# Optimization experiments

Hardware: AMD Instinct MI355X
Metric: run time of the kernel (lower is better)

The kernel has to match this reference:

```python
import jax, jax.numpy as jnp
import numpy as np

WEIGHT = 0.1  # init weight

# 6-connectivity (scipy generate_binary_structure(3,1)) neighbor reductions

def _nmin(x, fill):
    p = jnp.pad(x, 1, constant_values=fill)
    return jnp.minimum(
        jnp.minimum(jnp.minimum(p[:-2, 1:-1, 1:-1], p[2:, 1:-1, 1:-1]),
                    jnp.minimum(p[1:-1, :-2, 1:-1], p[1:-1, 2:, 1:-1])),
        jnp.minimum(p[1:-1, 1:-1, :-2], p[1:-1, 1:-1, 2:]))


def _nor(x):
    p = jnp.pad(x, 1, constant_values=False)
    return (p[:-2, 1:-1, 1:-1] | p[2:, 1:-1, 1:-1] |
            p[1:-1, :-2, 1:-1] | p[1:-1, 2:, 1:-1] |
            p[1:-1, 1:-1, :-2] | p[1:-1, 1:-1, 2:])


def _nand(x):
    # border_value=0 in scipy.binary_erosion -> pad with False
    p = jnp.pad(x, 1, constant_values=False)
    return (p[:-2, 1:-1, 1:-1] & p[2:, 1:-1, 1:-1] &
            p[1:-1, :-2, 1:-1] & p[1:-1, 2:, 1:-1] &
            p[1:-1, 1:-1, :-2] & p[1:-1, 1:-1, 2:])


def _cc_count(mask):
    # connected-component count via min-label propagation (6-connectivity),
    # equivalent to scipy.ndimage.label(...)[1]
    n = mask.size
    idx = jnp.arange(n, dtype=jnp.int32).reshape(mask.shape)
    big = jnp.int32(n)
    lbl0 = jnp.where(mask, idx, big)

    def body(c):
        lbl, _ = c
        new = jnp.where(mask, jnp.minimum(lbl, _nmin(lbl, big)), big)
        return new, jnp.any(new != lbl)

    lbl, _ = jax.lax.while_loop(lambda c: c[1], body, (lbl0, jnp.bool_(True)))
    # roots: voxels whose label equals their own index
    return jnp.sum(mask & (lbl == idx)).astype(jnp.int32)


def _cavity_volume(mask):
    # binary_fill_holes: background not reachable from the border
    bg = ~mask
    border = jnp.ones(mask.shape, bool).at[1:-1, 1:-1, 1:-1].set(False)
    r0 = bg & border

    def body(c):
        r, _ = c
        new = bg & (r | _nor(r))
        return new, jnp.any(new != r)

    reach, _ = jax.lax.while_loop(lambda c: c[1], body, (r0, jnp.bool_(True)))
    return jnp.sum(bg & ~reach).astype(jnp.int32)


def _betti(mask):
    b0 = _cc_count(mask)
    eroded = mask & _nand(mask)  # binary_erosion, iterations=1
    b0e = _cc_count(eroded)
    b1 = jnp.maximum(jnp.int32(0), b0 - b0e)
    b2 = _cavity_volume(mask) // 100
    return jnp.stack([b0, b1, b2]).astype(jnp.float32)


def setup_inputs() -> dict:
    key = jax.random.key(0)
    k1, k2 = jax.random.split(key)
    B, C, D, H, W = 2, 4, 64, 128, 128
    pred = jax.random.normal(k1, (B, C, D, H, W), dtype=jnp.float32)
    target = jax.random.randint(k2, (B, D, H, W), 0, C, dtype=jnp.int32)
    return {"pred": pred, "target": target}


def reference(pred, target):
    B, C = pred.shape[0], pred.shape[1]
    vol = pred.shape[2:]
    prob = jax.nn.softmax(pred, axis=1)
    # foreground classes 1..C-1, flattened to [B*(C-1), D, H, W]
    pred_masks = (prob[:, 1:] > 0.5).reshape((-1,) + vol)
    cls = jnp.arange(1, C, dtype=target.dtype).reshape(1, C - 1, 1, 1, 1)
    tgt_masks = (target[:, None] == cls).reshape((-1,) + vol)
    pb = jax.vmap(_betti)(pred_masks)  # [B*(C-1), 3]
    tb = jax.vmap(_betti)(tgt_masks)
    count = B * (C - 1)
    return WEIGHT * jnp.abs(pb - tb).sum() / count
```

## Files before the change

kernel.cpp:

```cpp
#include <hip/hip_runtime.h>
#include <stdint.h>

#define DD 64
#define HH 128
#define WW 128
#define NVOX (DD * HH * WW)
#define NWRD (NVOX / 32)
#define BATCH 2
#define NCLS 4
#define NMASK 12
#define NPROB 36
#define NTILE 128
#define MAXC 2048
#define VNODE (NTILE * MAXC)
#define NODE_STRIDE (VNODE + 64)
#define NTASKW 7424

__device__ __forceinline__ int uf_find(int* P, int x) {
    while (true) {
        int p = P[x];
        if (p == x) return x;
        int gp = P[p];
        if (gp != p) P[x] = gp;
        x = gp;
    }
}
__device__ __forceinline__ int uf_find_ro(const int* P, int x) {
    int p;
    while ((p = P[x]) != x) x = p;
    return x;
}
__device__ __forceinline__ void uf_union(int* P, int a, int b) {
    while (true) {
        a = uf_find(P, a);
        b = uf_find(P, b);
        if (a == b) return;
        int lo = a < b ? a : b;
        int hi = a < b ? b : a;
        int old = atomicCAS(&P[hi], hi, lo);
        if (old == hi) return;
        a = lo; b = old;
    }
}

#define SW(v) ((v) + ((v) >> 5))
__device__ __forceinline__ int lfind(int* lp, int x) {
    while (true) {
        int p = lp[SW(x)];
        if (p == x) return x;
        int gp = lp[SW(p)];
        if (gp != p) lp[SW(x)] = gp;
        x = gp;
    }
}
__device__ __forceinline__ void lunion(int* lp, int a, int b) {
    while (true) {
        a = lfind(lp, a);
        b = lfind(lp, b);
        if (a == b) return;
        int lo = a < b ? a : b;
        int hi = a < b ? b : a;
        int old = atomicCAS(&lp[SW(hi)], hi, lo);
        if (old == hi) return;
        a = lo; b = old;
    }
}
__device__ __forceinline__ int lresolve(const int* lp, int h) {
    int v = lp[SW(h)];
    while (v >= 0) v = lp[SW(v)];
    return -v - 1;
}
__device__ __forceinline__ int run_head(uint32_t w, int p) {
    uint32_t below = ~w & ((1u << p) - 1u);
    return below ? (32 - __clz((int)below)) : 0;
}

__device__ __forceinline__ uint32_t ld_word(const uint32_t* __restrict__ maskW,
                                            const uint32_t* __restrict__ erodW,
                                            int phase, int m, int w) {
    if (phase == 0) return maskW[m * NWRD + w];
    if (phase == 1) return erodW[m * NWRD + w];
    return ~maskW[m * NWRD + w];
}


__global__ void k_masks2(const float* __restrict__ pred, const int* __restrict__ tgt,
                         uint32_t* __restrict__ maskW, int* __restrict__ counts) {
    int tid = blockIdx.x * blockDim.x + threadIdx.x;
    if (tid < 64) counts[tid] = 0;
    int b = tid >> 20;
    int i = tid & (NVOX - 1);
    const float* p = pred + (size_t)b * NCLS * NVOX + i;
    float x0 = p[0], x1 = p[NVOX], x2 = p[2 * NVOX], x3 = p[3 * NVOX];
    float mx = fmaxf(fmaxf(x0, x1), fmaxf(x2, x3));
    float e0 = __expf(x0 - mx), e1 = __expf(x1 - mx), e2 = __expf(x2 - mx), e3 = __expf(x3 - mx);
    float S = e0 + e1 + e2 + e3;
    int t = tgt[(size_t)b * NVOX + i];
    int lane = threadIdx.x & 63;
    int wbase = i >> 5;
    float ev[3] = {e1, e2, e3};
    for (int c = 0; c < 3; ++c) {
        unsigned long long bal = __ballot(ev[c] / S > 0.5f);
        uint32_t* M = maskW + (size_t)(b * 3 + c) * NWRD;
        if (lane == 0)  M[wbase] = (uint32_t)bal;
        if (lane == 32) M[wbase] = (uint32_t)(bal >> 32);
        unsigned long long balT = __ballot(t == c + 1);
        uint32_t* MT = maskW + (size_t)(6 + b * 3 + c) * NWRD;
        if (lane == 0)  MT[wbase] = (uint32_t)balT;
        if (lane == 32) MT[wbase] = (uint32_t)(balT >> 32);
    }
}

__global__ void k_erode(const uint32_t* __restrict__ maskW, uint32_t* __restrict__ erodW) {
    int tid = blockIdx.x * blockDim.x + threadIdx.x;
    int m = tid / NWRD;
    int w = tid - m * NWRD;
    const uint32_t* M = maskW + (size_t)m * NWRD;
    int z = w >> 9, y = (w >> 2) & 127, q = w & 3;
    uint32_t a = M[w];
    uint32_t xl = (a << 1) | (q ? (M[w - 1] >> 31) : 0u);
    uint32_t xr = (a >> 1) | (q < 3 ? (M[w + 1] << 31) : 0u);
    uint32_t ym = (y > 0)   ? M[w - 4]   : 0u;
    uint32_t yp = (y < 127) ? M[w + 4]   : 0u;
    uint32_t zm = (z > 0)   ? M[w - 512] : 0u;
    uint32_t zp = (z < 63)  ? M[w + 512] : 0u;
    erodW[tid] = a & xl & xr & ym & yp & zm & zp;
}

__global__ void k_local(const uint32_t* __restrict__ maskW, const uint32_t* __restrict__ erodW,
                        uint16_t* __restrict__ C16all, int* __restrict__ Pall,
                        uint16_t* __restrict__ volAll, int* __restrict__ tcount,
                        int m0, int mb) {
    __shared__ int lp[8448];
    __shared__ uint32_t aw[256];
    __shared__ uint32_t lvol[MAXC / 2];
    __shared__ int lcount;
    int bid = blockIdx.x;
    int tile = bid / mb;
    int slot = bid - tile * mb;
    int pr = m0 + slot;
    int phase = pr / 12, m = pr % 12;
    uint16_t* C16 = C16all + (size_t)slot * NVOX;
    int* P = Pall + (size_t)slot * NODE_STRIDE;
    int tz = tile >> 4, ty = tile & 15;
    int t2 = threadIdx.x;
    int wl = t2 >> 1;
    int h  = t2 & 1;
    int zl = wl >> 5, yl = (wl >> 2) & 7, q = wl & 3;
    int gw = ((tz * 8 + zl) * 128 + (ty * 8 + yl)) * 4 + q;
    uint32_t afull = ld_word(maskW, erodW, phase, m, gw);
    if (h == 0) aw[wl] = afull;
    uint32_t a16 = (afull >> (16 * h)) & 0xFFFFu;
    if (t2 == 0) lcount = 0;
    if (tile == 0 && t2 == 0) P[VNODE] = VNODE;

    int lbase = t2 << 4;
    uint32_t heads = a16 & ~(a16 << 1) & 0xFFFFu;
    {
        uint32_t st = heads;
        while (st) { int p = __ffs(st) - 1; st &= st - 1; lp[SW(lbase + p)] = lbase + p; }
    }
    __syncthreads();

    if (a16) {
        if (a16 & 1u) {
            if (h == 1) {
                uint32_t lo16 = afull & 0xFFFFu;
                if (lo16 >> 15) lunion(lp, lbase, lbase - 16 + run_head(lo16, 15));
            } else if (q) {
                uint32_t hi16 = aw[wl - 1] >> 16;
                if (hi16 >> 15) lunion(lp, lbase, lbase - 16 + run_head(hi16, 15));
            }
        }
        if (yl < 7) {
            uint32_t by = (aw[wl + 4] >> (16 * h)) & 0xFFFFu;
            uint32_t ov = a16 & by;
            uint32_t st = ov & ~(ov << 1);
            int la = -1, lb = -1;
            while (st) {
                int p = __ffs(st) - 1; st &= st - 1;
                int ha = lbase + run_head(a16, p);
                int hb = lbase + 128 + run_head(by, p);
                if (ha != la || hb != lb) { lunion(lp, ha, hb); la = ha; lb = hb; }
            }
        }
        if (zl < 7) {
            uint32_t bz = (aw[wl + 32] >> (16 * h)) & 0xFFFFu;
            uint32_t ov = a16 & bz;
            uint32_t st = ov & ~(ov << 1);
            int la = -1, lb = -1;
            while (st) {
                int p = __ffs(st) - 1; st &= st - 1;
                int ha = lbase + run_head(a16, p);
                int hb = lbase + 1024 + run_head(bz, p);
                if (ha != la || hb != lb) { lunion(lp, ha, hb); la = ha; lb = hb; }
            }
        }
    }
    __syncthreads();

    if (phase == 2) { lvol[t2] = 0; lvol[t2 + 512] = 0; }

    int tileBase = tile * MAXC;
    {
        uint32_t st = heads;
        while (st) {
            int p = __ffs(st) - 1; st &= st - 1;
            int hh = lbase + p;
            if (lp[SW(hh)] == hh) {
                int k = atomicAdd(&lcount, 1);
                lp[SW(hh)] = -k - 1;
                P[tileBase + k] = tileBase + k;
            }
        }
    }
    __syncthreads();

    if (t2 == 0) tcount[slot * NTILE + tile] = lcount;

    bool faceRow = (yl == 0 || yl == 7 || zl == 0 || zl == 7);
    if (a16 && (phase == 2 || faceRow)) {
        int i0 = (gw << 5) + 16 * h;
        int gz = tz * 8 + zl, gy = ty * 8 + yl;
        bool bordRow = (phase == 2) && (gz == 0 || gz == 63 || gy == 0 || gy == 127);
        if (faceRow && a16 == 0xFFFFu) {
            int id = lresolve(lp, lbase);
            uint32_t pk = (uint32_t)id * 0x10001u;
            uint4 v = make_uint4(pk, pk, pk, pk);
            uint4* dst = (uint4*)(C16 + i0);
            dst[0] = v; dst[1] = v;
            if (phase == 2) {
                atomicAdd(&lvol[id >> 1], 16u << ((id & 1) * 16));
                if (bordRow || (q == 0 && h == 0) || (q == 3 && h == 1))
                    P[tileBase + id] = VNODE;
            }
        } else {
            int htop = (a16 >> 15) ? run_head(a16, 15) : -1;
            uint32_t st = heads;
            while (st) {
                int p = __ffs(st) - 1; st &= st - 1;
                int id = lresolve(lp, lbase + p);
                uint32_t run = a16 >> p;
                int len = __ffs(~run) - 1;
                if (faceRow) {
                    C16[i0 + p] = (uint16_t)id;
                    for (int j = 1; j < len; ++j) C16[i0 + p + j] = (uint16_t)id;
                }
                if (phase == 2) {
                    atomicAdd(&lvol[id >> 1], (uint32_t)len << ((id & 1) * 16));
                    if (bordRow || (q == 0 && h == 0 && p == 0) ||
                        (q == 3 && h == 1 && p == htop))
                        P[tileBase + id] = VNODE;
                }
            }
        }
    }
    __syncthreads();

    if (phase == 2) {
        uint16_t* volC = volAll + (size_t)slot * (NTILE * MAXC) + tileBase;
        for (int k = t2; k < lcount; k += 512)
            volC[k] = (uint16_t)((lvol[k >> 1] >> ((k & 1) * 16)) & 0xFFFFu);
    }
}

__global__ void k_bmerge(const uint32_t* __restrict__ maskW, const uint32_t* __restrict__ erodW,
                         const uint16_t* __restrict__ C16all, int* __restrict__ Pall,
                         int m0) {
    int t = blockIdx.x * blockDim.x + threadIdx.x;
    int slot = blockIdx.y;
    int pr = m0 + slot;
    int phase = pr / 12, m = pr % 12;
    bool act = (t < NTASKW);

    int w = 0, dw = 4, dv = WW, tA = 0, tB = 0;
    if (act) {
        if (t < 3840) {
            int q = t & 3, r = t >> 2;
            int yi = r >> 6, z = r & 63;
            int y = 8 * yi + 7;
            w = (z * 128 + y) * 4 + q;
            dw = 4; dv = WW;
            tA = ((z >> 3) * 16 + yi) * MAXC;
            tB = tA + MAXC;
        } else {
            int tt = t - 3840;
            int q = tt & 3, r = tt >> 2;
            int zi = r >> 7, y = r & 127;
            int z = 8 * zi + 7;
            w = (z * 128 + y) * 4 + q;
            dw = 512; dv = HH * WW;
            tA = (zi * 16 + (y >> 3)) * MAXC;
            tB = tA + 16 * MAXC;
        }
    }

    uint32_t ov = 0;
    if (act) {
        uint32_t a = ld_word(maskW, erodW, phase, m, w);
        if (a) {
            uint32_t b = ld_word(maskW, erodW, phase, m, w + dw);
            ov = a & b;
        }
    }

    const uint16_t* C16 = C16all + (size_t)slot * NVOX;
    int* P = Pall + (size_t)slot * NODE_STRIDE;
    int i0 = w << 5;
    uint32_t st = ov & ~(ov << 1);

    int ca = -1, cb = -1, p0 = -1;
    if (st) {
        p0 = __ffs(st) - 1;
        ca = tA + C16[i0 + p0];
        cb = tB + C16[i0 + p0 + dv];
    }
    int la = __shfl_up(ca, 1);
    int lb = __shfl_up(cb, 1);
    if ((threadIdx.x & 63) == 0) { la = -1; lb = -1; }

    while (st) {
        int p = __ffs(st) - 1; st &= st - 1;
        int xa, xb;
        if (p == p0) { xa = ca; xb = cb; }
        else { xa = tA + C16[i0 + p]; xb = tB + C16[i0 + p + dv]; }
        if (xa != la || xb != lb) { uf_union(P, xa, xb); la = xa; lb = xb; }
    }
}

__global__ void k_flatc(const int* __restrict__ Pall, const uint16_t* __restrict__ volAll,
                        const int* __restrict__ tcount, int* __restrict__ counts, int m0) {
    __shared__ int sAcc;
    __shared__ int sRootV;
    int slot = blockIdx.y;
    int pr = m0 + slot;
    int phase = pr / 12;
    int tile = blockIdx.x;
    const int* P = Pall + (size_t)slot * NODE_STRIDE;
    int lc = tcount[slot * NTILE + tile];
    if (threadIdx.x == 0) {
        sAcc = 0;
        sRootV = (phase == 2) ? uf_find_ro(P, VNODE) : 0;
    }
    __syncthreads();
    int cnt = 0;
    if (phase == 2) {
        const uint16_t* volC = volAll + (size_t)slot * (NTILE * MAXC) + tile * MAXC;
        int rootV = sRootV;
        for (int k = threadIdx.x; k < lc; k += blockDim.x) {
            int id = tile * MAXC + k;
            if (uf_find_ro(P, id) != rootV) cnt += volC[k];
        }
    } else {
        for (int k = threadIdx.x; k < lc; k += blockDim.x) {
            int id = tile * MAXC + k;
            if (uf_find_ro(P, id) == id) ++cnt;
        }
    }
    for (int off = 32; off; off >>= 1) cnt += __shfl_down(cnt, off);
    if ((threadIdx.x & 63) == 0 && cnt) atomicAdd(&sAcc, cnt);
    __syncthreads();
    if (threadIdx.x == 0 && sAcc) atomicAdd(&counts[pr], sAcc);
}

__global__ void k_loss(const int* __restrict__ counts, float* __restrict__ out) {
    if (threadIdx.x != 0 || blockIdx.x != 0) return;
    float acc = 0.f;
    for (int m = 0; m < 6; ++m) {
        int pb0 = counts[m],      pbe = counts[12 + m],      pcv = counts[24 + m];
        int tb0 = counts[6 + m],  tbe = counts[12 + 6 + m],  tcv = counts[24 + 6 + m];
        int pb1 = max(0, pb0 - pbe), tb1 = max(0, tb0 - tbe);
        int pb2 = pcv / 100, tb2 = tcv / 100;
        acc += fabsf((float)(pb0 - tb0)) + fabsf((float)(pb1 - tb1)) + fabsf((float)(pb2 - tb2));
    }
    out[0] = 0.1f * acc / 6.0f;
}

extern "C" void kernel_launch(void* const* d_in, const int* in_sizes, int n_in,
                              void* d_out, int out_size, void* d_ws, size_t ws_size,
                              hipStream_t stream) {
    const float* pred = (const float*)d_in[0];
    const int* tgt = (const int*)d_in[1];
    float* out = (float*)d_out;

    uint8_t* ws = (uint8_t*)d_ws;
    uint32_t* maskW = (uint32_t*)ws;
    size_t off = (size_t)NMASK * NWRD * 4;
    uint32_t* erodW = (uint32_t*)(ws + off);
    off += (size_t)NMASK * NWRD * 4;
    int* counts = (int*)(ws + off);
    off += 256;
    int* tcount = (int*)(ws + off);
    off += (size_t)NPROB * NTILE * 4;
    off = (off + 255) & ~(size_t)255;

    size_t avail = ws_size > off ? ws_size - off : 0;
    size_t slot_bytes = (size_t)NVOX * 2 + (size_t)NODE_STRIDE * 4
                      + (size_t)NTILE * MAXC * 2;
    int PB = (int)(avail / slot_bytes);
    if (PB > NPROB) PB = NPROB;
    if (PB < 1) PB = 1;

    uint16_t* C16all = (uint16_t*)(ws + off);
    int* Pall = (int*)(ws + off + (size_t)PB * NVOX * 2);
    uint16_t* volAll = (uint16_t*)(ws + off + (size_t)PB * NVOX * 2
                                   + (size_t)PB * NODE_STRIDE * 4);

    k_masks2<<<dim3((BATCH * NVOX) / 256), 256, 0, stream>>>(pred, tgt, maskW, counts);
    k_erode<<<dim3((NMASK * NWRD) / 256), 256, 0, stream>>>(maskW, erodW);

    for (int m0 = 0; m0 < NPROB; m0 += PB) {
        int mb = PB < (NPROB - m0) ? PB : (NPROB - m0);
        k_local <<<dim3(NTILE * mb), 512, 0, stream>>>(maskW, erodW, C16all, Pall,
                                                       volAll, tcount, m0, mb);
        k_bmerge<<<dim3((NTASKW + 255) / 256, mb), 256, 0, stream>>>(maskW, erodW, C16all,
                                                                     Pall, m0);
        k_flatc <<<dim3(NTILE, mb), 256, 0, stream>>>(Pall, volAll, tcount, counts, m0);
    }

    k_loss<<<1, 64, 0, stream>>>(counts, out);
}
```

Measured before the change: 227.6 us.

## Use wave-level aggregation for local root labeling and volume atomics

Root allocation in the per-tile labeling kernel now uses one wave-level prefix scan and a single shared atomic per wave, replacing one atomic per root. Cavity volume accumulation takes a fast path when every lane in a wave holds the same component: it reduces across the wave and issues one shared atomic. Otherwise it falls back to per-lane or per-run atomics. The grid is also reordered so tiles run along x and problem slots along y, which changes block scheduling order. The cost is extra shuffles and ballots, and a second pass over runs for lanes that span several components.

```diff
diff --git a/kernel.cpp b/kernel.cpp
--- a/kernel.cpp
+++ b/kernel.cpp
@@ -129,21 +129,20 @@
 
 __global__ void k_local(const uint32_t* __restrict__ maskW, const uint32_t* __restrict__ erodW,
                         uint16_t* __restrict__ C16all, int* __restrict__ Pall,
-                        uint16_t* __restrict__ volAll, int* __restrict__ tcount,
-                        int m0, int mb) {
+                        uint16_t* __restrict__ volAll, int* __restrict__ tcount, int m0) {
     __shared__ int lp[8448];
     __shared__ uint32_t aw[256];
     __shared__ uint32_t lvol[MAXC / 2];
     __shared__ int lcount;
-    int bid = blockIdx.x;
-    int tile = bid / mb;
-    int slot = bid - tile * mb;
+    int slot = blockIdx.y;
     int pr = m0 + slot;
     int phase = pr / 12, m = pr % 12;
     uint16_t* C16 = C16all + (size_t)slot * NVOX;
     int* P = Pall + (size_t)slot * NODE_STRIDE;
+    int tile = blockIdx.x;
     int tz = tile >> 4, ty = tile & 15;
     int t2 = threadIdx.x;
+    int lane = t2 & 63;
     int wl = t2 >> 1;
     int h  = t2 & 1;
     int zl = wl >> 5, yl = (wl >> 2) & 7, q = wl & 3;
@@ -203,21 +202,37 @@
 
     int tileBase = tile * MAXC;
     {
+        uint32_t rootMask = 0; int nr = 0;
         uint32_t st = heads;
         while (st) {
             int p = __ffs(st) - 1; st &= st - 1;
             int hh = lbase + p;
-            if (lp[SW(hh)] == hh) {
-                int k = atomicAdd(&lcount, 1);
-                lp[SW(hh)] = -k - 1;
-                P[tileBase + k] = tileBase + k;
-            }
+            if (lp[SW(hh)] == hh) { rootMask |= 1u << p; ++nr; }
+        }
+        int pre = nr;
+        for (int off = 1; off < 64; off <<= 1) {
+            int v = __shfl_up(pre, off);
+            if (lane >= off) pre += v;
+        }
+        int waveTot = __shfl(pre, 63);
+        int base = 0;
+        if (lane == 63 && waveTot) base = atomicAdd(&lcount, waveTot);
+        base = __shfl(base, 63);
+        int k = base + pre - nr;
+        st = rootMask;
+        while (st) {
+            int p = __ffs(st) - 1; st &= st - 1;
+            int hh = lbase + p;
+            lp[SW(hh)] = -k - 1;
+            P[tileBase + k] = tileBase + k;
+            ++k;
         }
     }
     __syncthreads();
 
     if (t2 == 0) tcount[slot * NTILE + tile] = lcount;
 
+    int myId = -1, myLen = 0; bool multi = false;
     bool faceRow = (yl == 0 || yl == 7 || zl == 0 || zl == 7);
     if (a16 && (phase == 2 || faceRow)) {
         int i0 = (gw << 5) + 16 * h;
@@ -230,7 +245,7 @@
             uint4* dst = (uint4*)(C16 + i0);
             dst[0] = v; dst[1] = v;
             if (phase == 2) {
-                atomicAdd(&lvol[id >> 1], 16u << ((id & 1) * 16));
+                myId = id; myLen = 16;
                 if (bordRow || (q == 0 && h == 0) || (q == 3 && h == 1))
                     P[tileBase + id] = VNODE;
             }
@@ -247,10 +262,41 @@
                     for (int j = 1; j < len; ++j) C16[i0 + p + j] = (uint16_t)id;
                 }
                 if (phase == 2) {
-                    atomicAdd(&lvol[id >> 1], (uint32_t)len << ((id & 1) * 16));
+                    if (myLen == 0) myId = id;
+                    else if (id != myId) multi = true;
+                    myLen += len;
                     if (bordRow || (q == 0 && h == 0 && p == 0) ||
                         (q == 3 && h == 1 && p == htop))
                         P[tileBase + id] = VNODE;
+                }
+            }
+        }
+    }
+
+    if (phase == 2) {
+        unsigned long long hasMask = __ballot(myLen > 0);
+        if (hasMask) {
+            bool anyMulti = __any(multi);
+            int firstLane = __ffsll(hasMask) - 1;
+            int leadId = __shfl(myId, firstLane);
+            bool uni = !anyMulti && __all(myLen == 0 || myId == leadId);
+            if (uni) {
+                int s = myLen;
+                for (int off = 32; off; off >>= 1) s += __shfl_down(s, off);
+                if (lane == 0 && s)
+                    atomicAdd(&lvol[leadId >> 1], (uint32_t)s << ((leadId & 1) * 16));
+            } else if (myLen > 0) {
+                if (!multi) {
+                    atomicAdd(&lvol[myId >> 1], (uint32_t)myLen << ((myId & 1) * 16));
+                } else {
+                    uint32_t st = heads;
+                    while (st) {
+                        int p = __ffs(st) - 1; st &= st - 1;
+                        int id = lresolve(lp, lbase + p);
+                        uint32_t run = a16 >> p;
+                        int len = __ffs(~run) - 1;
+                        atomicAdd(&lvol[id >> 1], (uint32_t)len << ((id & 1) * 16));
+                    }
                 }
             }
         }
@@ -411,8 +457,8 @@
 
     for (int m0 = 0; m0 < NPROB; m0 += PB) {
         int mb = PB < (NPROB - m0) ? PB : (NPROB - m0);
-        k_local <<<dim3(NTILE * mb), 512, 0, stream>>>(maskW, erodW, C16all, Pall,
-                                                       volAll, tcount, m0, mb);
+        k_local <<<dim3(NTILE, mb), 512, 0, stream>>>(maskW, erodW, C16all, Pall,
+                                                      volAll, tcount, m0);
         k_bmerge<<<dim3((NTASKW + 255) / 256, mb), 256, 0, stream>>>(maskW, erodW, C16all,
                                                                      Pall, m0);
         k_flatc <<<dim3(NTILE, mb), 256, 0, stream>>>(Pall, volAll, tcount, counts, m0);
```

After: 217.9 us. 1.04x faster.
